# Performance work log

Measured on AMD Instinct MI355X. Metric: run time of the kernel, lower is better.

Reference implementation:

```python
import jax, jax.numpy as jnp
import numpy as np

QMIN, QMAX = -128.0, 127.0


def fake_quantize(x, scale, zero_point):
    # quantize->dequantize (int8 cast in torch only clips; values already integral)
    q = jnp.clip(jnp.round(x / scale) + zero_point, QMIN, QMAX)
    return (q - zero_point) * scale


def _bk_resolvent_diag(he_diag, h0_super, h0_sub, z):
    """Diagonal of G = (z - H)^{-1} for tridiagonal H via two continued-fraction sweeps.
    he_diag: (B, N) float32; h0_super/h0_sub: (N-1,) float32; z: complex scalar.
    Returns (B, N) complex64.
    """
    a = he_diag.astype(jnp.complex64).T          # (N, B)
    c = (h0_sub * h0_super).astype(jnp.complex64)  # (N-1,) coupling b_i * c_i
    Bsz = a.shape[1]
    zero = jnp.zeros((Bsz,), jnp.complex64)

    def step(carry, inp):
        ai, ci = inp
        new = ci / (z - ai - carry)
        return new, new

    # Left sweep: L_0 = 0, L_i = c_{i-1} / (z - a_{i-1} - L_{i-1})
    _, Lrest = jax.lax.scan(step, zero, (a[:-1], c))
    L = jnp.concatenate([zero[None], Lrest], axis=0)          # (N, B)
    # Right sweep: R_{N-1} = 0, R_i = c_i / (z - a_{i+1} - R_{i+1})
    _, Rrest = jax.lax.scan(step, zero, (a[1:][::-1], c[::-1]))
    R = jnp.concatenate([zero[None], Rrest], axis=0)[::-1]     # (N, B)

    G = 1.0 / (z - a - L - R)                                   # (N, B)
    return G.T


def setup_inputs() -> dict:
    key = jax.random.key(0)
    B, N = 512, 16384
    v_fp32 = jax.random.normal(key, (B, N), dtype=jnp.float32)
    h0_diag = jnp.full((N,), -2.0, dtype=jnp.float32)
    h0_sub = jnp.ones((N - 1,), dtype=jnp.float32)
    h0_super = jnp.ones((N - 1,), dtype=jnp.float32)
    return {"v_fp32": v_fp32, "h0_diag": h0_diag, "h0_sub": h0_sub, "h0_super": h0_super}


def reference(v_fp32, h0_diag, h0_sub, h0_super):
    # fake-quantize the potential (training path, scale=1.0, zp=0 defaults)
    v = fake_quantize(v_fp32, jnp.float32(1.0), jnp.float32(0.0))
    he_diag = jnp.clip(h0_diag[None, :] + v, -10.0, 10.0)       # (B, N)
    z = jnp.complex64(1j)
    G = _bk_resolvent_diag(he_diag, h0_super, h0_sub, z)        # (B, N) complex
    G_real = jnp.clip(G.real.astype(jnp.float32), -100.0, 100.0)
    G_imag = jnp.clip(G.imag.astype(jnp.float32), -100.0, 100.0)
    G_real = fake_quantize(G_real, jnp.float32(1.0), jnp.float32(0.0))
    G_imag = fake_quantize(G_imag, jnp.float32(1.0), jnp.float32(0.0))
    return jnp.stack([G_real, G_imag], axis=-1)                 # (B, N, 2)
```

## Files before the change

kernel.cpp:

```cpp
#include <hip/hip_runtime.h>


#define SEG    16
#define WCHEAP 16
#define WEXACT 8
#define WARM   (WCHEAP + WEXACT)
#define LANES  64
#define WAVES  4
#define NTHR   (LANES * WAVES)
#define CHUNK  (LANES*SEG)
#define BCHUNK (WAVES * CHUNK)
#define HALO   WARM
#define BSTAGE (BCHUNK + 2*HALO)
#define SPAD   (BSTAGE + BSTAGE/32 + 1)

struct C2 { float r, i; };

__device__ __forceinline__ int padi(int i) { return i + (i >> 5); }

__device__ __forceinline__ float fdiv_ieee(float num, float den) {
  const float r0 = __builtin_amdgcn_rcpf(den);
  const float e0 = __builtin_fmaf(-den, r0, 1.0f);
  const float r1 = __builtin_fmaf(e0, r0, r0);
  const float q0 = num * r1;
  const float e1 = __builtin_fmaf(-den, q0, num);
  const float q1 = __builtin_fmaf(e1, r1, q0);
  const float e2 = __builtin_fmaf(-den, q1, num);
  return __builtin_fmaf(e2, r1, q1);
}

__device__ __forceinline__ C2 npdiv(float nr, float dr, float di) {
  #pragma clang fp contract(off)
  const bool  b   = fabsf(dr) >= fabsf(di);
  const float num = b ? di : dr;
  const float den = b ? dr : di;
  const float rat = fdiv_ieee(num, den);
  const float t   = num * rat;
  const float s   = den + t;
  const float scl = fdiv_ieee(1.0f, s);
  const float u   = nr * scl;
  const float m   = nr * rat;
  const float w   = m * scl;
  C2 o;
  o.r = b ? u : w;
  o.i = b ? -w : -u;
  return o;
}

__device__ __forceinline__ void cf_step(float na, float cv, float& cr, float& ci) {
  #pragma clang fp contract(off)
  const float dr = na - cr;
  const float di = 1.0f - ci;
  const C2 nc = npdiv(cv, dr, di);
  cr = nc.r; ci = nc.i;
}

__device__ __forceinline__ void cf_cheap(float na, float cv, float& cr, float& ci) {
  const float dr = na - cr;
  const float di = 1.0f - ci;
  const float m2 = dr * dr + di * di;
  const float r  = __builtin_amdgcn_rcpf(m2);
  const float t  = cv * r;
  cr = dr * t;
  ci = -(di * t);
}

__device__ __forceinline__ float neg_a(float vv, float hd) {
  #pragma clang fp contract(off)
  float q = rintf(vv);
  q = fminf(fmaxf(q, -128.0f), 127.0f);
  float he = hd + q;
  he = fminf(fmaxf(he, -10.0f), 10.0f);
  return 0.0f - he;
}

__device__ __forceinline__ float fq_out(float x) {
  #pragma clang fp contract(off)
  x = fminf(fmaxf(x, -100.0f), 100.0f);
  x = rintf(x);
  x = fminf(fmaxf(x, -128.0f), 127.0f);
  return x;
}

__global__ void cc_kernel(const float* __restrict__ hsub,
                          const float* __restrict__ hsup,
                          float* __restrict__ ccf, int N) {
  #pragma clang fp contract(off)
  const int i = blockIdx.x * blockDim.x + threadIdx.x;
  if (i < N + 2*HALO + 8) {
    const int k = i - HALO;
    ccf[i] = (k >= 0 && k < N - 1) ? hsub[k] * hsup[k] : 0.0f;
  }
}

__device__ __forceinline__ void load8_f(const float4* __restrict__ cc4,
                                        int m0, float* w) {
  const int q = (m0 + HALO) >> 2;
  const float4 A = cc4[q];
  const float4 B = cc4[q + 1];
  w[0]=A.x; w[1]=A.y; w[2]=A.z; w[3]=A.w;
  w[4]=B.x; w[5]=B.y; w[6]=B.z; w[7]=B.w;
}

__device__ __forceinline__ void load8_b(const float4* __restrict__ cc4,
                                        int m0, float* w) {
  const int q = (m0 + HALO - 3) >> 2;
  const float4 A = cc4[q];
  const float4 B = cc4[q + 1];
  const float4 C = cc4[q + 2];
  w[0]=A.w;
  w[1]=B.x; w[2]=B.y; w[3]=B.z; w[4]=B.w;
  w[5]=C.x; w[6]=C.y; w[7]=C.z;
}

__global__ void __launch_bounds__(NTHR)
bk_kernel(const float* __restrict__ v,
          const float* __restrict__ hdiag,
          const float* __restrict__ ccf,
          float2* __restrict__ out,
          int N, int chunks_per_row, int blocks_per_row) {
  #pragma clang fp contract(off)
  __shared__ float sA[SPAD];

  const int tid  = threadIdx.x;
  const int lane = tid & (LANES - 1);
  const int wv   = tid >> 6;
  const int row  = blockIdx.x / blocks_per_row;
  const int cb   = blockIdx.x - row * blocks_per_row;
  const int bbase = cb * BCHUNK;
  const long rowoff = (long)row * N;
  const float4* cc4 = (const float4*)ccf;

  for (int i = tid; i < BSTAGE; i += NTHR) {
    const int k = bbase - HALO + i;
    float na = 0.0f;
    if (k >= 0 && k < N) na = neg_a(v[rowoff + k], hdiag[k]);
    sA[padi(i)] = na;
  }
  __syncthreads();

  const int chunk = cb * WAVES + wv;
  if (chunk < chunks_per_row) {
    const int base = bbase + wv * CHUNK;
    const int s0  = base + lane * SEG;
    const int s1  = s0 + SEG;
    const int loff = bbase - HALO;
    const int li0 = s0 - loff;

    float Rr[SEG], Ri[SEG];
    float crB, ciB;
    float crF, ciF;
    float wcB[8], wcF[8];

    crB = 0.0f; ciB = 0.0f; crF = 0.0f; ciF = 0.0f;
    #pragma unroll
    for (int g = 0; g < WARM / 8; ++g) {
      const int kh = s1 + (WARM - 1) - 8 * g;
      const int kl = s0 - WARM + 8 * g;
      load8_b(cc4, kh - 8, wcB);
      load8_f(cc4, kl, wcF);
      #pragma unroll
      for (int j = 0; j < 8; ++j) {
        const float naB = sA[padi(kh - j - loff)];
        const float naF = sA[padi(kl + j - loff)];
        if (g < (WCHEAP / 8)) {
          cf_cheap(naB, wcB[7 - j], crB, ciB);
          cf_cheap(naF, wcF[j],     crF, ciF);
        } else {
          cf_step(naB, wcB[7 - j], crB, ciB);
          cf_step(naF, wcF[j],     crF, ciF);
        }
      }
    }
    Rr[SEG-1] = crB; Ri[SEG-1] = ciB;

    #pragma unroll
    for (int tg = 0; tg < SEG / 8; ++tg) {
      const int th = SEG - 1 - 8 * tg;
      load8_b(cc4, s0 + th - 8, wcB);
      #pragma unroll
      for (int j = 0; j < 8; ++j) {
        const int t = th - j;
        if (t >= 1) {
          const float na = sA[padi(li0 + t)];
          cf_step(na, wcB[7 - j], crB, ciB);
          Rr[t-1] = crB; Ri[t-1] = ciB;
        }
      }
    }

    #pragma unroll
    for (int tg = 0; tg < SEG / 8; ++tg) {
      const int kl = s0 + 8 * tg;
      load8_f(cc4, kl, wcF);
      #pragma unroll
      for (int j = 0; j < 8; ++j) {
        const int t = 8 * tg + j;
        const float na  = sA[padi(li0 + t)];
        const float drL = na - crF;
        const float diL = 1.0f - ciF;
        const float drf = drL - Rr[t];
        const float dif = diL - Ri[t];
        const C2 G = npdiv(1.0f, drf, dif);
        out[rowoff + kl + j] = make_float2(fq_out(G.r), fq_out(G.i));
        if (t < SEG - 1) {
          const C2 nc = npdiv(wcF[j], drL, diL);
          crF = nc.r; ciF = nc.i;
        }
      }
    }
  }
}

extern "C" void kernel_launch(void* const* d_in, const int* in_sizes, int n_in,
                              void* d_out, int out_size, void* d_ws, size_t ws_size,
                              hipStream_t stream) {
  const float* v    = (const float*)d_in[0];
  const float* hd   = (const float*)d_in[1];
  const float* hsub = (const float*)d_in[2];
  const float* hsup = (const float*)d_in[3];
  const int N = in_sizes[1];
  const int B = in_sizes[0] / N;
  const int chunks = (N + CHUNK - 1) / CHUNK;
  const int bpr    = (chunks + WAVES - 1) / WAVES;

  float* ccf = (float*)d_ws;
  const int ccn = N + 2*HALO + 8;
  cc_kernel<<<(ccn + 255) / 256, 256, 0, stream>>>(hsub, hsup, ccf, N);
  bk_kernel<<<B * bpr, NTHR, 0, stream>>>(v, hd, ccf, (float2*)d_out,
                                          N, chunks, bpr);
}
```

Baseline: 124.1 us.

## Interleave forward and backward sweeps within segment and vectorize output stores

Restructures the per-thread segment computation so the forward (left) and backward (right) continued-fraction recurrences run interleaved. Each half of the segment is finished by whichever sweep reaches it second, which roughly halves the length of the serial dependency chain and gives the scheduler two independent chains to overlap. Outputs are buffered in registers and written as float4 stores instead of scalar float2 stores. In exchange the code needs more live registers and more complex indexing.

```diff
diff --git a/kernel.cpp b/kernel.cpp
--- a/kernel.cpp
+++ b/kernel.cpp
@@ -2,6 +2,7 @@
 
 
 #define SEG    16
+#define HSEG   (SEG/2)
 #define WCHEAP 16
 #define WEXACT 8
 #define WARM   (WCHEAP + WEXACT)
@@ -147,7 +148,7 @@
     const int loff = bbase - HALO;
     const int li0 = s0 - loff;
 
-    float Rr[SEG], Ri[SEG];
+    float Ar[HSEG], Ai[HSEG], Br[HSEG], Bi[HSEG];
     float crB, ciB;
     float crF, ciF;
     float wcB[8], wcF[8];
@@ -172,42 +173,66 @@
         }
       }
     }
-    Rr[SEG-1] = crB; Ri[SEG-1] = ciB;
-
-    #pragma unroll
-    for (int tg = 0; tg < SEG / 8; ++tg) {
-      const int th = SEG - 1 - 8 * tg;
-      load8_b(cc4, s0 + th - 8, wcB);
-      #pragma unroll
-      for (int j = 0; j < 8; ++j) {
-        const int t = th - j;
-        if (t >= 1) {
-          const float na = sA[padi(li0 + t)];
-          cf_step(na, wcB[7 - j], crB, ciB);
-          Rr[t-1] = crB; Ri[t-1] = ciB;
-        }
+    Br[HSEG-1] = crB; Bi[HSEG-1] = ciB;
+
+    float w0[8], w1[8];
+    load8_f(cc4, s0,     w0);
+    load8_f(cc4, s0 + 8, w1);
+
+    #pragma unroll
+    for (int k = 0; k < 8; ++k) {
+      Ar[k] = crF; Ai[k] = ciF;
+      const float naF = sA[padi(li0 + k)];
+      const float drL = naF - crF;
+      const float diL = 1.0f - ciF;
+      { const C2 nc = npdiv(w0[k], drL, diL); crF = nc.r; ciF = nc.i; }
+      if (k < 7) {
+        const float naB = sA[padi(li0 + 15 - k)];
+        cf_step(naB, w1[6 - k], crB, ciB);
+        Br[6 - k] = crB; Bi[6 - k] = ciB;
       }
     }
 
     #pragma unroll
-    for (int tg = 0; tg < SEG / 8; ++tg) {
-      const int kl = s0 + 8 * tg;
-      load8_f(cc4, kl, wcF);
-      #pragma unroll
-      for (int j = 0; j < 8; ++j) {
-        const int t = 8 * tg + j;
-        const float na  = sA[padi(li0 + t)];
-        const float drL = na - crF;
-        const float diL = 1.0f - ciF;
-        const float drf = drL - Rr[t];
-        const float dif = diL - Ri[t];
-        const C2 G = npdiv(1.0f, drf, dif);
-        out[rowoff + kl + j] = make_float2(fq_out(G.r), fq_out(G.i));
-        if (t < SEG - 1) {
-          const C2 nc = npdiv(wcF[j], drL, diL);
-          crF = nc.r; ciF = nc.i;
-        }
+    for (int k = 0; k < 8; ++k) {
+      const int t = 8 + k;
+      const float naD = sA[padi(li0 + t)];
+      const float drLD = naD - crF;
+      const float diLD = 1.0f - ciF;
+      const float drfD = drLD - Br[k];
+      const float difD = diLD - Bi[k];
+      const C2 GD = npdiv(1.0f, drfD, difD);
+      if (k < 7) {
+        const C2 nc = npdiv(w1[k], drLD, diLD);
+        crF = nc.r; ciF = nc.i;
       }
+      Br[k] = fq_out(GD.r); Bi[k] = fq_out(GD.i);
+      const int u = 7 - k;
+      const float naS = sA[padi(li0 + u + 1)];
+      cf_step(naS, w0[u], crB, ciB);
+      const float naG = sA[padi(li0 + u)];
+      const float drLG = naG - Ar[u];
+      const float diLG = 1.0f - Ai[u];
+      const float drfG = drLG - crB;
+      const float difG = diLG - ciB;
+      const C2 GG = npdiv(1.0f, drfG, difG);
+      Ar[u] = fq_out(GG.r); Ai[u] = fq_out(GG.i);
+    }
+
+    float4* op = (float4*)(&out[rowoff + s0]);
+    #pragma unroll
+    for (int q = 0; q < 4; ++q) {
+      float4 f4;
+      f4.x = Ar[2*q];     f4.y = Ai[2*q];
+      f4.z = Ar[2*q + 1]; f4.w = Ai[2*q + 1];
+      op[q] = f4;
+    }
+    #pragma unroll
+    for (int q = 0; q < 4; ++q) {
+      float4 f4;
+      f4.x = Br[2*q];     f4.y = Bi[2*q];
+      f4.z = Br[2*q + 1]; f4.w = Bi[2*q + 1];
+      op[4 + q] = f4;
     }
   }
 }
```

Measured after the change: 134.5 us. 8.4% more time.
